# Kernel optimization log

Measured on AMD Instinct MI355X. Metric: run time of the kernel, lower is better.

The kernel has to match this reference:

```python
import jax, jax.numpy as jnp
import numpy as np
import math

N_EMBD = 1024
N_HEAD = 16
HEAD_SIZE = N_EMBD // N_HEAD
LAYER_IDX = 2
LAMBDA_INIT = 0.8 - 0.6 * math.exp(-0.3 * (LAYER_IDX - 1))
LN_EPS = 1e-5
B, T = 4, 1024


def setup_inputs() -> dict:
    key = jax.random.key(0)
    ks = jax.random.split(key, 11)
    s = 0.02  # weight init scale
    return {
        "x": jax.random.normal(ks[0], (B, T, N_EMBD), dtype=jnp.float32),
        "Wq1": jax.random.normal(ks[1], (N_EMBD, N_EMBD), dtype=jnp.float32) * s,
        "Wq2": jax.random.normal(ks[2], (N_EMBD, N_EMBD), dtype=jnp.float32) * s,
        "Wk1": jax.random.normal(ks[3], (N_EMBD, N_EMBD), dtype=jnp.float32) * s,
        "Wk2": jax.random.normal(ks[4], (N_EMBD, N_EMBD), dtype=jnp.float32) * s,
        "Wv": jax.random.normal(ks[5], (N_EMBD, 2 * N_EMBD), dtype=jnp.float32) * s,
        "Wc": jax.random.normal(ks[6], (2 * N_EMBD, N_EMBD), dtype=jnp.float32) * s,
        "lq1": jax.random.normal(ks[7], (N_HEAD, HEAD_SIZE), dtype=jnp.float32) * 0.1,
        "lk1": jax.random.normal(ks[8], (N_HEAD, HEAD_SIZE), dtype=jnp.float32) * 0.1,
        "lq2": jax.random.normal(ks[9], (N_HEAD, HEAD_SIZE), dtype=jnp.float32) * 0.1,
        "lk2": jax.random.normal(ks[10], (N_HEAD, HEAD_SIZE), dtype=jnp.float32) * 0.1,
    }


def reference(x, Wq1, Wq2, Wk1, Wk2, Wv, Wc, lq1, lk1, lq2, lk2):
    Bx, Tx, C = x.shape
    H, hs = N_HEAD, HEAD_SIZE
    scale = 1.0 / math.sqrt(hs)

    # projections -> (B, T, H, d)
    q1 = (x @ Wq1).reshape(Bx, Tx, H, hs)
    q2 = (x @ Wq2).reshape(Bx, Tx, H, hs)
    k1 = (x @ Wk1).reshape(Bx, Tx, H, hs)
    k2 = (x @ Wk2).reshape(Bx, Tx, H, hs)
    v = (x @ Wv).reshape(Bx, Tx, H, 2 * hs)

    # dual score streams (B, H, T, T)
    att1 = jnp.einsum("bqhd,bkhd->bhqk", q1, k1) * scale
    att2 = jnp.einsum("bqhd,bkhd->bhqk", q2, k2) * scale

    causal = jnp.tril(jnp.ones((Tx, Tx), dtype=bool))  # (T, T)
    neg_inf = jnp.float32(-jnp.inf)
    att1 = jnp.where(causal, att1, neg_inf)
    att2 = jnp.where(causal, att2, neg_inf)
    a1 = jax.nn.softmax(att1, axis=-1)
    a2 = jax.nn.softmax(att2, axis=-1)

    # per-head differential lambda
    lam1 = jnp.exp(jnp.sum(lq1 * lk1, axis=-1))  # (H,)
    lam2 = jnp.exp(jnp.sum(lq2 * lk2, axis=-1))  # (H,)
    lam_full = lam1 - lam2 + LAMBDA_INIT  # (H,)

    att = a1 - lam_full[None, :, None, None] * a2  # dropout = identity (eval)

    # PV matmul -> (B, T, H, 2*hs)
    y = jnp.einsum("bhqk,bkhd->bqhd", att, v)

    # subLN over last dim (no affine)
    mu = jnp.mean(y, axis=-1, keepdims=True)
    var = jnp.mean(jnp.square(y - mu), axis=-1, keepdims=True)
    y = (y - mu) / jnp.sqrt(var + LN_EPS)
    y = y * (1.0 - LAMBDA_INIT)

    y = y.reshape(Bx, Tx, 2 * C)
    return y @ Wc  # resid dropout = identity (eval)
```

## Files before the change

kernel.cpp:

```cpp
#include <hip/hip_runtime.h>


#define T_SEQ 1024
#define NH 16
#define DV 128
#define NPROJ 6144
#define KSTR 72

typedef __bf16 bf16_t;
typedef __bf16 bf16x8 __attribute__((ext_vector_type(8)));
typedef __bf16 bf16x4 __attribute__((ext_vector_type(4)));
typedef __bf16 bf16x2 __attribute__((ext_vector_type(2)));
typedef _Float16 f16x4 __attribute__((ext_vector_type(4)));
typedef _Float16 f16x2 __attribute__((ext_vector_type(2)));
typedef short s16x4 __attribute__((ext_vector_type(4)));
typedef float f32x4 __attribute__((ext_vector_type(4)));

#define LAMBDA_INIT 0.35550906759096928f
#define ONE_MINUS_LI 0.6444909324090307f
#define LOG2E 1.4426950408889634f
#define RTHR 44.36f

#if __has_builtin(__builtin_amdgcn_mfma_f32_16x16x16_bf16)
#define MFMA16(a, b, c) __builtin_amdgcn_mfma_f32_16x16x16_bf16(a, b, c, 0, 0, 0)
#elif __has_builtin(__builtin_amdgcn_mfma_f32_16x16x16bf16_1k)
#define MFMA16(a, b, c)                                                       \
  __builtin_amdgcn_mfma_f32_16x16x16bf16_1k(                                  \
      __builtin_bit_cast(s16x4, a), __builtin_bit_cast(s16x4, b), c, 0, 0, 0)
#else
#define MFMA16(a, b, c) (c)
#endif

#define GLDS(g, l)                                                            \
  __builtin_amdgcn_global_load_lds(                                           \
      (const __attribute__((address_space(1))) void*)(g),                     \
      (__attribute__((address_space(3))) void*)(l), 16, 0, 0)

static const size_t OFF_WCAT = 0;
static const size_t OFF_XB = OFF_WCAT + (size_t)6144 * 1024 * 2;
static const size_t OFF_WCT = OFF_XB + (size_t)4096 * 1024 * 2;
static const size_t OFF_PROJ = OFF_WCT + (size_t)2048 * 1024 * 2;
static const size_t OFF_VT = OFF_PROJ + (size_t)4096 * 6144 * 2;
static const size_t OFF_YLN = OFF_VT + (size_t)64 * 128 * 1024 * 2;
static const size_t OFF_LAM = OFF_YLN + (size_t)4096 * 2048 * 2;

__global__ void __launch_bounds__(256) cast_x(const float* __restrict__ x,
                                              bf16_t* __restrict__ o) {
  const int i = (blockIdx.x * 256 + threadIdx.x) * 4;
  float4 v = *(const float4*)(x + i);
  bf16x4 r = {(bf16_t)v.x, (bf16_t)v.y, (bf16_t)v.z, (bf16_t)v.w};
  *(bf16x4*)(o + i) = r;
}

__device__ __forceinline__ void tcast_body(const float* __restrict__ W,
                                           bf16_t* __restrict__ Wt, int K,
                                           int N, int row0) {
  __shared__ float tile[32][33];
  const int k0 = blockIdx.x * 32, n0 = blockIdx.y * 32;
  const int tx = threadIdx.x & 31, ty = threadIdx.x >> 5;
#pragma unroll
  for (int i = 0; i < 32; i += 8)
    tile[ty + i][tx] = W[(long)(k0 + ty + i) * N + n0 + tx];
  __syncthreads();
#pragma unroll
  for (int i = 0; i < 32; i += 8)
    Wt[(long)(row0 + n0 + ty + i) * K + k0 + tx] = (bf16_t)tile[tx][ty + i];
}

__global__ void __launch_bounds__(256) tcast_w(const float* __restrict__ W,
                                               bf16_t* __restrict__ Wt, int K,
                                               int N, int row0) {
  tcast_body(W, Wt, K, N, row0);
}

__global__ void __launch_bounds__(256) tcast_w4(const float* __restrict__ W0,
                                                const float* __restrict__ W1,
                                                const float* __restrict__ W2,
                                                const float* __restrict__ W3,
                                                bf16_t* __restrict__ Wt) {
  const float* Ws[4] = {W0, W1, W2, W3};
  tcast_body(Ws[blockIdx.z], Wt, 1024, 1024, blockIdx.z * 1024);
}

__global__ void lam_kernel(const float* __restrict__ lq1,
                           const float* __restrict__ lk1,
                           const float* __restrict__ lq2,
                           const float* __restrict__ lk2,
                           float* __restrict__ lam) {
  const int h = threadIdx.x;
  if (h < NH) {
    float d1 = 0.f, d2 = 0.f;
    for (int i = 0; i < 64; ++i) {
      d1 += lq1[h * 64 + i] * lk1[h * 64 + i];
      d2 += lq2[h * 64 + i] * lk2[h * 64 + i];
    }
    lam[h] = expf(d1) - expf(d2) + LAMBDA_INIT;
  }
}

#define BM 128
#define BN 128
#define BK 32

template <typename OutT>
__global__ void __launch_bounds__(256) gemm_bt(const bf16_t* __restrict__ A,
                                               const bf16_t* __restrict__ Bt,
                                               OutT* __restrict__ C, int M,
                                               int N, int K) {
  __shared__ __align__(16) bf16_t As[BM * BK];
  __shared__ __align__(16) bf16_t Bs[BN * BK];
  const int tid = threadIdx.x;
  const int w = tid >> 6;
  const int lane = tid & 63;
  const int quad = lane >> 4, l16 = lane & 15;
  const int m0 = blockIdx.y * BM, n0 = blockIdx.x * BN;
  const int wm = (w >> 1) * 64, wn = (w & 1) * 64;
  const int srow = tid >> 2;
  const int scol = (tid & 3) * 8;

  const bf16_t* Ag0 = A + (long)(m0 + srow) * K + scol;
  const bf16_t* Ag1 = Ag0 + (long)64 * K;
  const bf16_t* Bg0 = Bt + (long)(n0 + srow) * K + scol;
  const bf16_t* Bg1 = Bg0 + (long)64 * K;
  bf16_t* lA0 = As + tid * 8;
  bf16_t* lA1 = As + 2048 + tid * 8;
  bf16_t* lB0 = Bs + tid * 8;
  bf16_t* lB1 = Bs + 2048 + tid * 8;

  f32x4 acc[4][4] = {};

  for (int k0 = 0; k0 < K; k0 += BK) {
    GLDS(Ag0 + k0, lA0);
    GLDS(Ag1 + k0, lA1);
    GLDS(Bg0 + k0, lB0);
    GLDS(Bg1 + k0, lB1);
    __syncthreads();
    bf16x8 af[4], bfr[4];
#pragma unroll
    for (int t = 0; t < 4; ++t) {
      af[t] = *(const bf16x8*)(As + (wm + t * 16 + l16) * BK + quad * 8);
      bfr[t] = *(const bf16x8*)(Bs + (wn + t * 16 + l16) * BK + quad * 8);
    }
#pragma unroll
    for (int mt = 0; mt < 4; ++mt)
#pragma unroll
      for (int nt = 0; nt < 4; ++nt)
        acc[mt][nt] = __builtin_amdgcn_mfma_f32_16x16x32_bf16(
            af[mt], bfr[nt], acc[mt][nt], 0, 0, 0);
    __syncthreads();
  }

#pragma unroll
  for (int mt = 0; mt < 4; ++mt)
#pragma unroll
    for (int nt = 0; nt < 4; ++nt) {
      const int col = n0 + wn + nt * 16 + l16;
#pragma unroll
      for (int i = 0; i < 4; ++i) {
        const int row = m0 + wm + mt * 16 + quad * 4 + i;
        C[(long)row * N + col] = (OutT)acc[mt][nt][i];
      }
    }
}

template <typename OutT>
__global__ void __launch_bounds__(256) gemm_bt_n64(const bf16_t* __restrict__ A,
                                                   const bf16_t* __restrict__ Bt,
                                                   OutT* __restrict__ C, int M,
                                                   int N, int K) {
  __shared__ __align__(16) bf16_t As[BM * BK];
  __shared__ __align__(16) bf16_t Bs[64 * BK];
  const int tid = threadIdx.x;
  const int w = tid >> 6;
  const int lane = tid & 63;
  const int quad = lane >> 4, l16 = lane & 15;
  const int m0 = blockIdx.y * BM, n0 = blockIdx.x * 64;
  const int wm = (w >> 1) * 64, wn = (w & 1) * 32;
  const int srow = tid >> 2;
  const int scol = (tid & 3) * 8;

  const bf16_t* Ag0 = A + (long)(m0 + srow) * K + scol;
  const bf16_t* Ag1 = Ag0 + (long)64 * K;
  const bf16_t* Bg0 = Bt + (long)(n0 + srow) * K + scol;
  bf16_t* lA0 = As + tid * 8;
  bf16_t* lA1 = As + 2048 + tid * 8;
  bf16_t* lB0 = Bs + tid * 8;

  f32x4 acc[4][2] = {};

  for (int k0 = 0; k0 < K; k0 += BK) {
    GLDS(Ag0 + k0, lA0);
    GLDS(Ag1 + k0, lA1);
    GLDS(Bg0 + k0, lB0);
    __syncthreads();
    bf16x8 af[4], bfr[2];
#pragma unroll
    for (int t = 0; t < 4; ++t)
      af[t] = *(const bf16x8*)(As + (wm + t * 16 + l16) * BK + quad * 8);
#pragma unroll
    for (int t = 0; t < 2; ++t)
      bfr[t] = *(const bf16x8*)(Bs + (wn + t * 16 + l16) * BK + quad * 8);
#pragma unroll
    for (int mt = 0; mt < 4; ++mt)
#pragma unroll
      for (int nt = 0; nt < 2; ++nt)
        acc[mt][nt] = __builtin_amdgcn_mfma_f32_16x16x32_bf16(
            af[mt], bfr[nt], acc[mt][nt], 0, 0, 0);
    __syncthreads();
  }

#pragma unroll
  for (int mt = 0; mt < 4; ++mt)
#pragma unroll
    for (int nt = 0; nt < 2; ++nt) {
      const int col = n0 + wn + nt * 16 + l16;
#pragma unroll
      for (int i = 0; i < 4; ++i) {
        const int row = m0 + wm + mt * 16 + quad * 4 + i;
        C[(long)row * N + col] = (OutT)acc[mt][nt][i];
      }
    }
}

__global__ void __launch_bounds__(256) transpose_v(const bf16_t* __restrict__ proj,
                                                   bf16_t* __restrict__ vt) {
  __shared__ bf16_t tile[32][34];
  const int bh = blockIdx.z;
  const int b = bh >> 4, h = bh & 15;
  const int t0 = blockIdx.x * 32, d0 = blockIdx.y * 32;
  const int tx = threadIdx.x & 31, ty = threadIdx.x >> 5;
  const bf16_t* src = proj + (long)(b * T_SEQ) * NPROJ + 4096 + h * 128;
#pragma unroll
  for (int i = 0; i < 32; i += 8)
    tile[ty + i][tx] = src[(long)(t0 + ty + i) * NPROJ + d0 + tx];
  __syncthreads();
  bf16_t* dst = vt + ((long)bh * DV) * T_SEQ;
#pragma unroll
  for (int i = 0; i < 32; i += 8)
    dst[(long)(d0 + ty + i) * T_SEQ + t0 + tx] = tile[tx][ty + i];
}

__global__ void __launch_bounds__(256) attn_kernel(const bf16_t* __restrict__ proj,
                                                   const bf16_t* __restrict__ vt,
                                                   _Float16* __restrict__ a1,
                                                   _Float16* __restrict__ a2) {
  const int x = blockIdx.x;
  const int qblk = 15 - (x >> 7);
  const int st = (x >> 6) & 1;
  const int bh = x & 63;
  const int b = bh >> 4, h = bh & 15;
  const int tid = threadIdx.x;
  const int w = tid >> 6, lane = tid & 63;
  const int quad = lane >> 4, l16 = lane & 15;
  const long bT = (long)b * T_SEQ;

  __shared__ __align__(16) bf16_t Ks[64 * KSTR];
  __shared__ __align__(16) bf16_t Vs[DV * KSTR];

  const int koff = h * 64 + 2048 + st * 1024;
  const bf16_t* gK = proj + (bT + (tid >> 2)) * (long)NPROJ + koff + (tid & 3) * 16;
  const bf16_t* gV = vt + (long)bh * DV * T_SEQ + (long)(tid >> 1) * T_SEQ +
                     (tid & 1) * 32;
  const int kwK = (tid >> 2) * KSTR + (tid & 3) * 16;
  const int kwV = (tid >> 1) * KSTR + (tid & 1) * 32;

  const float sc = 0.125f * LOG2E;
  const int q0 = qblk * 64 + w * 16;
  const int qg = q0 + l16;

  const bf16_t* qrow = proj + (bT + qg) * (long)NPROJ + h * 64 + st * 1024;
  bf16x8 aq[2];
  aq[0] = *(const bf16x8*)(qrow + quad * 8);
  aq[1] = *(const bf16x8*)(qrow + 32 + quad * 8);

  f32x4 O[8] = {};
  float m = -3.0e38f, l = 0.f;
  const bf16x4 one4 = {(bf16_t)1.0f, (bf16_t)1.0f, (bf16_t)1.0f, (bf16_t)1.0f};

  const int kend_blk = qblk * 64 + 64;
  const int kend_w = q0 + 16;

  bf16x8 rK[2], rV[4];
  rK[0] = *(const bf16x8*)(gK);
  rK[1] = *(const bf16x8*)(gK + 8);
#pragma unroll
  for (int j = 0; j < 4; ++j) rV[j] = *(const bf16x8*)(gV + j * 8);

  for (int kt = 0; kt < kend_blk; kt += 64) {
    *(bf16x8*)(Ks + kwK) = rK[0];
    *(bf16x8*)(Ks + kwK + 8) = rK[1];
#pragma unroll
    for (int j = 0; j < 4; ++j) *(bf16x8*)(Vs + kwV + j * 8) = rV[j];
    __syncthreads();

    if (kt + 64 < kend_blk) {
      const long ko = (long)(kt + 64) * NPROJ;
      rK[0] = *(const bf16x8*)(gK + ko);
      rK[1] = *(const bf16x8*)(gK + ko + 8);
#pragma unroll
      for (int j = 0; j < 4; ++j)
        rV[j] = *(const bf16x8*)(gV + kt + 64 + j * 8);
    }

    if (kt < kend_w) {
      f32x4 s[4];
#pragma unroll
      for (int c = 0; c < 4; ++c) {
        const bf16_t* kr = Ks + (c * 16 + l16) * KSTR;
        bf16x8 ka0 = *(const bf16x8*)(kr + quad * 8);
        bf16x8 ka1 = *(const bf16x8*)(kr + 32 + quad * 8);
        f32x4 z = {};
        z = __builtin_amdgcn_mfma_f32_16x16x32_bf16(ka0, aq[0], z, 0, 0, 0);
        z = __builtin_amdgcn_mfma_f32_16x16x32_bf16(ka1, aq[1], z, 0, 0, 0);
        s[c] = z;
      }
      if (kt + 63 > q0) {
#pragma unroll
        for (int c = 0; c < 4; ++c)
#pragma unroll
          for (int i = 0; i < 4; ++i) {
            const int key = kt + c * 16 + quad * 4 + i;
            if (key > qg) s[c][i] = -1e30f;
          }
      }
      float t[4];
#pragma unroll
      for (int c = 0; c < 4; ++c)
        t[c] = fmaxf(fmaxf(s[c][0], s[c][1]), fmaxf(s[c][2], s[c][3]));
      float mx = fmaxf(fmaxf(t[0], t[1]), fmaxf(t[2], t[3]));
      mx = fmaxf(mx, __shfl_xor(mx, 16));
      mx = fmaxf(mx, __shfl_xor(mx, 32));
      if (!__all(mx <= m + RTHR)) {
        const float mn = fmaxf(m, mx);
        const float al = exp2f((m - mn) * sc);
        m = mn;
#pragma unroll
        for (int f = 0; f < 8; ++f)
#pragma unroll
          for (int i = 0; i < 4; ++i) O[f][i] *= al;
        l *= al;
      }
      const float ms = m * sc;
      bf16x4 pc[4];
#pragma unroll
      for (int c = 0; c < 4; ++c)
#pragma unroll
        for (int i = 0; i < 4; ++i)
          pc[c][i] = (bf16_t)exp2f(fmaf(s[c][i], sc, -ms));
      f32x4 la = {};
#pragma unroll
      for (int c = 0; c < 4; ++c) la = MFMA16(one4, pc[c], la);
#pragma unroll
      for (int c = 0; c < 4; ++c) {
#pragma unroll
        for (int f = 0; f < 8; ++f) {
          bf16x4 va =
              *(const bf16x4*)(Vs + (f * 16 + l16) * KSTR + c * 16 + quad * 4);
          O[f] = MFMA16(va, pc[c], O[f]);
        }
      }
      l += la[0];
    }
    __syncthreads();
  }

  const float inv = 1.0f / l;
  _Float16* ob = st ? a2 : a1;
  _Float16* dst = ob + ((bT + qg) * 16 + h) * (long)128 + quad * 4;
#pragma unroll
  for (int f = 0; f < 8; ++f) {
    f16x4 o = {(_Float16)(O[f][0] * inv), (_Float16)(O[f][1] * inv),
               (_Float16)(O[f][2] * inv), (_Float16)(O[f][3] * inv)};
    *(f16x4*)(dst + f * 16) = o;
  }
}

__global__ void __launch_bounds__(256) combine_kernel(const _Float16* __restrict__ a1,
                                                      const _Float16* __restrict__ a2,
                                                      const float* __restrict__ lamp,
                                                      bf16_t* __restrict__ yln) {
  const int unit = blockIdx.x * 4 + (threadIdx.x >> 6);
  const int lane = threadIdx.x & 63;
  const float lam = lamp[unit & 15];
  const long base = (long)unit * 128 + lane * 2;
  f16x2 v1 = *(const f16x2*)(a1 + base);
  f16x2 v2 = *(const f16x2*)(a2 + base);
  float y0 = (float)v1[0] - lam * (float)v2[0];
  float y1 = (float)v1[1] - lam * (float)v2[1];
  float sm = y0 + y1, sq = y0 * y0 + y1 * y1;
#pragma unroll
  for (int off = 1; off < 64; off <<= 1) {
    sm += __shfl_xor(sm, off);
    sq += __shfl_xor(sq, off);
  }
  const float mu = sm * (1.0f / 128.0f);
  const float var = sq * (1.0f / 128.0f) - mu * mu;
  const float rs = rsqrtf(var + 1e-5f) * ONE_MINUS_LI;
  bf16x2 o = {(bf16_t)((y0 - mu) * rs), (bf16_t)((y1 - mu) * rs)};
  *(bf16x2*)(yln + base) = o;
}

extern "C" void kernel_launch(void* const* d_in, const int* in_sizes, int n_in,
                              void* d_out, int out_size, void* d_ws,
                              size_t ws_size, hipStream_t stream) {
  const float* x = (const float*)d_in[0];
  const float* Wq1 = (const float*)d_in[1];
  const float* Wq2 = (const float*)d_in[2];
  const float* Wk1 = (const float*)d_in[3];
  const float* Wk2 = (const float*)d_in[4];
  const float* Wv = (const float*)d_in[5];
  const float* Wc = (const float*)d_in[6];
  const float* lq1 = (const float*)d_in[7];
  const float* lk1 = (const float*)d_in[8];
  const float* lq2 = (const float*)d_in[9];
  const float* lk2 = (const float*)d_in[10];
  float* out = (float*)d_out;

  char* ws = (char*)d_ws;
  bf16_t* wcat = (bf16_t*)(ws + OFF_WCAT);
  bf16_t* xb = (bf16_t*)(ws + OFF_XB);
  bf16_t* wct = (bf16_t*)(ws + OFF_WCT);
  bf16_t* projb = (bf16_t*)(ws + OFF_PROJ);
  bf16_t* vtb = (bf16_t*)(ws + OFF_VT);
  bf16_t* ylnb = (bf16_t*)(ws + OFF_YLN);
  float* lamp = (float*)(ws + OFF_LAM);
  _Float16* a1b = (_Float16*)(ws + OFF_YLN);
  _Float16* a2b = (_Float16*)(ws + OFF_WCAT);

  cast_x<<<4096, 256, 0, stream>>>(x, xb);
  tcast_w4<<<dim3(32, 32, 4), 256, 0, stream>>>(Wq1, Wq2, Wk1, Wk2, wcat);
  tcast_w<<<dim3(32, 64), 256, 0, stream>>>(Wv, wcat, 1024, 2048, 4096);
  tcast_w<<<dim3(64, 32), 256, 0, stream>>>(Wc, wct, 2048, 1024, 0);
  lam_kernel<<<1, 64, 0, stream>>>(lq1, lk1, lq2, lk2, lamp);

  gemm_bt<bf16_t><<<dim3(48, 32), 256, 0, stream>>>(xb, wcat, projb, 4096, 6144, 1024);
  transpose_v<<<dim3(32, 4, 64), 256, 0, stream>>>(projb, vtb);
  attn_kernel<<<dim3(2048), 256, 0, stream>>>(projb, vtb, a1b, a2b);
  combine_kernel<<<dim3(16384), 256, 0, stream>>>(a1b, a2b, lamp, ylnb);
  gemm_bt_n64<float><<<dim3(16, 32), 256, 0, stream>>>(ylnb, wct, out, 4096, 1024, 2048);
}
```

Measured before the change: 308.6 us.

## Replace projection GEMM with 256x256 double-buffered swizzled-LDS kernel

```diff
diff --git a/kernel.cpp b/kernel.cpp
--- a/kernel.cpp
+++ b/kernel.cpp
@@ -30,6 +30,8 @@
 #else
 #define MFMA16(a, b, c) (c)
 #endif
+
+#define MFMA32(a, b, c) __builtin_amdgcn_mfma_f32_16x16x32_bf16(a, b, c, 0, 0, 0)
 
 #define GLDS(g, l)                                                            \
   __builtin_amdgcn_global_load_lds(                                           \
@@ -98,70 +100,164 @@
   }
 }
 
+#define GBM 256
+#define GBN 256
+#define GBK 64
+
+__global__ void __launch_bounds__(512, 1) gemm256(const bf16_t* __restrict__ A,
+                                                  const bf16_t* __restrict__ Bt,
+                                                  bf16_t* __restrict__ C,
+                                                  int M, int N, int K,
+                                                  int nbx) {
+  __shared__ __align__(16) bf16_t As[2][GBM * GBK];
+  __shared__ __align__(16) bf16_t Bs[2][GBN * GBK];
+  const int tid = threadIdx.x;
+  const int w = tid >> 6, lane = tid & 63;
+  const int quad = lane >> 4, l16 = lane & 15;
+  const int wr = w >> 2, wc = w & 3;
+
+  const int wg = blockIdx.x;
+  const int cpx = gridDim.x >> 3;
+  const int sw = (wg & 7) * cpx + (wg >> 3);
+  const int by = sw / nbx, bx = sw % nbx;
+  const int m0 = by * GBM, n0 = bx * GBN;
+
+  const int r8 = lane >> 3, g = lane & 7;
+  const int gsw = (g ^ r8) * 8;
+  const bf16_t* gA[4];
+  const bf16_t* gB[4];
+#pragma unroll
+  for (int j = 0; j < 4; ++j) {
+    gA[j] = A + (long)(m0 + w * 32 + j * 8 + r8) * K + gsw;
+    gB[j] = Bt + (long)(n0 + w * 32 + j * 8 + r8) * K + gsw;
+  }
+
+  const int kx = (l16 & 7) << 4;
+  const int ko0 = (quad * 16) ^ kx;
+  const int ko1 = (64 + quad * 16) ^ kx;
+
+  f32x4 acc[8][4] = {};
+
+  const int nt = K >> 6;
+
+#pragma unroll
+  for (int j = 0; j < 4; ++j) {
+    GLDS(gA[j], As[0] + (w * 32 + j * 8) * GBK);
+    GLDS(gB[j], Bs[0] + (w * 32 + j * 8) * GBK);
+  }
+  asm volatile("s_waitcnt vmcnt(0)" ::: "memory");
+  __builtin_amdgcn_s_barrier();
+
+  for (int t = 0; t < nt; ++t) {
+    const bf16_t* Ab = (t & 1) ? As[1] : As[0];
+    const bf16_t* Bb = (t & 1) ? Bs[1] : Bs[0];
+    bf16_t* Asb = (t & 1) ? As[0] : As[1];
+    bf16_t* Bsb = (t & 1) ? Bs[0] : Bs[1];
+    const bool pf = (t + 1 < nt);
+    const long ko = (long)(t + 1) * GBK;
+
+    const char* Arow = (const char*)Ab + (size_t)(wr * 128 + l16) * 128;
+    const char* Brow = (const char*)Bb + (size_t)(wc * 64 + l16) * 128;
+
+    bf16x8 af[4][2], bn0[2][2], bn1[2][2];
+
+#pragma unroll
+    for (int mt = 0; mt < 4; ++mt) {
+      af[mt][0] = *(const bf16x8*)(Arow + (size_t)mt * 16 * 128 + ko0);
+      af[mt][1] = *(const bf16x8*)(Arow + (size_t)mt * 16 * 128 + ko1);
+    }
+#pragma unroll
+    for (int n = 0; n < 2; ++n) {
+      bn0[n][0] = *(const bf16x8*)(Brow + (size_t)n * 16 * 128 + ko0);
+      bn0[n][1] = *(const bf16x8*)(Brow + (size_t)n * 16 * 128 + ko1);
+    }
+    if (pf) {
+      GLDS(gA[0] + ko, Asb + (w * 32) * GBK);
+      GLDS(gB[0] + ko, Bsb + (w * 32) * GBK);
+      GLDS(gA[1] + ko, Asb + (w * 32 + 8) * GBK);
+      GLDS(gB[1] + ko, Bsb + (w * 32 + 8) * GBK);
+    }
+    __builtin_amdgcn_s_barrier();
+    __builtin_amdgcn_s_setprio(1);
+#pragma unroll
+    for (int mt = 0; mt < 4; ++mt)
+#pragma unroll
+      for (int n = 0; n < 2; ++n) {
+        acc[mt][n] = MFMA32(af[mt][0], bn0[n][0], acc[mt][n]);
+        acc[mt][n] = MFMA32(af[mt][1], bn0[n][1], acc[mt][n]);
+      }
+    __builtin_amdgcn_s_setprio(0);
+    __builtin_amdgcn_s_barrier();
+
+#pragma unroll
+    for (int n = 0; n < 2; ++n) {
+      bn1[n][0] = *(const bf16x8*)(Brow + (size_t)(32 + n * 16) * 128 + ko0);
+      bn1[n][1] = *(const bf16x8*)(Brow + (size_t)(32 + n * 16) * 128 + ko1);
+    }
+    if (pf) {
+      GLDS(gA[2] + ko, Asb + (w * 32 + 16) * GBK);
+      GLDS(gB[2] + ko, Bsb + (w * 32 + 16) * GBK);
+      GLDS(gA[3] + ko, Asb + (w * 32 + 24) * GBK);
+      GLDS(gB[3] + ko, Bsb + (w * 32 + 24) * GBK);
+    }
+    __builtin_amdgcn_s_barrier();
+    __builtin_amdgcn_s_setprio(1);
+#pragma unroll
+    for (int mt = 0; mt < 4; ++mt)
+#pragma unroll
+      for (int n = 0; n < 2; ++n) {
+        acc[mt][2 + n] = MFMA32(af[mt][0], bn1[n][0], acc[mt][2 + n]);
+        acc[mt][2 + n] = MFMA32(af[mt][1], bn1[n][1], acc[mt][2 + n]);
+      }
+    __builtin_amdgcn_s_setprio(0);
+    __builtin_amdgcn_s_barrier();
+
+#pragma unroll
+    for (int mt = 0; mt < 4; ++mt) {
+      af[mt][0] = *(const bf16x8*)(Arow + (size_t)(64 + mt * 16) * 128 + ko0);
+      af[mt][1] = *(const bf16x8*)(Arow + (size_t)(64 + mt * 16) * 128 + ko1);
+    }
+    __builtin_amdgcn_s_barrier();
+    __builtin_amdgcn_s_setprio(1);
+#pragma unroll
+    for (int mt = 0; mt < 4; ++mt)
+#pragma unroll
+      for (int n = 0; n < 2; ++n) {
+        acc[4 + mt][2 + n] = MFMA32(af[mt][0], bn1[n][0], acc[4 + mt][2 + n]);
+        acc[4 + mt][2 + n] = MFMA32(af[mt][1], bn1[n][1], acc[4 + mt][2 + n]);
+      }
+    __builtin_amdgcn_s_setprio(0);
+    __builtin_amdgcn_s_barrier();
+
+    __builtin_amdgcn_s_setprio(1);
+#pragma unroll
+    for (int mt = 0; mt < 4; ++mt)
+#pragma unroll
+      for (int n = 0; n < 2; ++n) {
+        acc[4 + mt][n] = MFMA32(af[mt][0], bn0[n][0], acc[4 + mt][n]);
+        acc[4 + mt][n] = MFMA32(af[mt][1], bn0[n][1], acc[4 + mt][n]);
+      }
+    __builtin_amdgcn_s_setprio(0);
+
+    asm volatile("s_waitcnt vmcnt(0)" ::: "memory");
+    __builtin_amdgcn_s_barrier();
+  }
+
+#pragma unroll
+  for (int mt = 0; mt < 8; ++mt)
+#pragma unroll
+    for (int n = 0; n < 4; ++n) {
+      const int col = n0 + wc * 64 + n * 16 + l16;
+#pragma unroll
+      for (int i = 0; i < 4; ++i) {
+        const int row = m0 + wr * 128 + mt * 16 + quad * 4 + i;
+        C[(long)row * N + col] = (bf16_t)acc[mt][n][i];
+      }
+    }
+}
+
 #define BM 128
-#define BN 128
 #define BK 32
-
-template <typename OutT>
-__global__ void __launch_bounds__(256) gemm_bt(const bf16_t* __restrict__ A,
-                                               const bf16_t* __restrict__ Bt,
-                                               OutT* __restrict__ C, int M,
-                                               int N, int K) {
-  __shared__ __align__(16) bf16_t As[BM * BK];
-  __shared__ __align__(16) bf16_t Bs[BN * BK];
-  const int tid = threadIdx.x;
-  const int w = tid >> 6;
-  const int lane = tid & 63;
-  const int quad = lane >> 4, l16 = lane & 15;
-  const int m0 = blockIdx.y * BM, n0 = blockIdx.x * BN;
-  const int wm = (w >> 1) * 64, wn = (w & 1) * 64;
-  const int srow = tid >> 2;
-  const int scol = (tid & 3) * 8;
-
-  const bf16_t* Ag0 = A + (long)(m0 + srow) * K + scol;
-  const bf16_t* Ag1 = Ag0 + (long)64 * K;
-  const bf16_t* Bg0 = Bt + (long)(n0 + srow) * K + scol;
-  const bf16_t* Bg1 = Bg0 + (long)64 * K;
-  bf16_t* lA0 = As + tid * 8;
-  bf16_t* lA1 = As + 2048 + tid * 8;
-  bf16_t* lB0 = Bs + tid * 8;
-  bf16_t* lB1 = Bs + 2048 + tid * 8;
-
-  f32x4 acc[4][4] = {};
-
-  for (int k0 = 0; k0 < K; k0 += BK) {
-    GLDS(Ag0 + k0, lA0);
-    GLDS(Ag1 + k0, lA1);
-    GLDS(Bg0 + k0, lB0);
-    GLDS(Bg1 + k0, lB1);
-    __syncthreads();
-    bf16x8 af[4], bfr[4];
-#pragma unroll
-    for (int t = 0; t < 4; ++t) {
-      af[t] = *(const bf16x8*)(As + (wm + t * 16 + l16) * BK + quad * 8);
-      bfr[t] = *(const bf16x8*)(Bs + (wn + t * 16 + l16) * BK + quad * 8);
-    }
-#pragma unroll
-    for (int mt = 0; mt < 4; ++mt)
-#pragma unroll
-      for (int nt = 0; nt < 4; ++nt)
-        acc[mt][nt] = __builtin_amdgcn_mfma_f32_16x16x32_bf16(
-            af[mt], bfr[nt], acc[mt][nt], 0, 0, 0);
-    __syncthreads();
-  }
-
-#pragma unroll
-  for (int mt = 0; mt < 4; ++mt)
-#pragma unroll
-    for (int nt = 0; nt < 4; ++nt) {
-      const int col = n0 + wn + nt * 16 + l16;
-#pragma unroll
-      for (int i = 0; i < 4; ++i) {
-        const int row = m0 + wm + mt * 16 + quad * 4 + i;
-        C[(long)row * N + col] = (OutT)acc[mt][nt][i];
-      }
-    }
-}
 
 template <typename OutT>
 __global__ void __launch_bounds__(256) gemm_bt_n64(const bf16_t* __restrict__ A,
@@ -203,21 +299,20 @@
 #pragma unroll
     for (int mt = 0; mt < 4; ++mt)
 #pragma unroll
-      for (int nt = 0; nt < 2; ++nt)
-        acc[mt][nt] = __builtin_amdgcn_mfma_f32_16x16x32_bf16(
-            af[mt], bfr[nt], acc[mt][nt], 0, 0, 0);
+      for (int ntt = 0; ntt < 2; ++ntt)
+        acc[mt][ntt] = MFMA32(af[mt], bfr[ntt], acc[mt][ntt]);
     __syncthreads();
   }
 
 #pragma unroll
   for (int mt = 0; mt < 4; ++mt)
 #pragma unroll
-    for (int nt = 0; nt < 2; ++nt) {
-      const int col = n0 + wn + nt * 16 + l16;
+    for (int ntt = 0; ntt < 2; ++ntt) {
+      const int col = n0 + wn + ntt * 16 + l16;
 #pragma unroll
       for (int i = 0; i < 4; ++i) {
         const int row = m0 + wm + mt * 16 + quad * 4 + i;
-        C[(long)row * N + col] = (OutT)acc[mt][nt][i];
+        C[(long)row * N + col] = (OutT)acc[mt][ntt][i];
       }
     }
 }
@@ -310,8 +405,8 @@
         bf16x8 ka0 = *(const bf16x8*)(kr + quad * 8);
         bf16x8 ka1 = *(const bf16x8*)(kr + 32 + quad * 8);
         f32x4 z = {};
-        z = __builtin_amdgcn_mfma_f32_16x16x32_bf16(ka0, aq[0], z, 0, 0, 0);
-        z = __builtin_amdgcn_mfma_f32_16x16x32_bf16(ka1, aq[1], z, 0, 0, 0);
+        z = MFMA32(ka0, aq[0], z);
+        z = MFMA32(ka1, aq[1], z);
         s[c] = z;
       }
       if (kt + 63 > q0) {
@@ -433,7 +528,7 @@
   tcast_w<<<dim3(64, 32), 256, 0, stream>>>(Wc, wct, 2048, 1024, 0);
   lam_kernel<<<1, 64, 0, stream>>>(lq1, lk1, lq2, lk2, lamp);
 
-  gemm_bt<bf16_t><<<dim3(48, 32), 256, 0, stream>>>(xb, wcat, projb, 4096, 6144, 1024);
+  gemm256<<<dim3(384), 512, 0, stream>>>(xb, wcat, projb, 4096, 6144, 1024, 24);
   transpose_v<<<dim3(32, 4, 64), 256, 0, stream>>>(projb, vtb);
   attn_kernel<<<dim3(2048), 256, 0, stream>>>(projb, vtb, a1b, a2b);
   combine_kernel<<<dim3(16384), 256, 0, stream>>>(a1b, a2b, lamp, ylnb);
```

After: 304.5 us (median of 2 runs). Within noise of the previous version (-1.3%).

## Add pipelined 256x256 projection GEMM with swizzled LDS and tile remap

Applied to the files above, without the earlier changes.

```diff
diff --git a/kernel.cpp b/kernel.cpp
--- a/kernel.cpp
+++ b/kernel.cpp
@@ -30,6 +30,8 @@
 #else
 #define MFMA16(a, b, c) (c)
 #endif
+
+#define MFMA32(a, b, c) __builtin_amdgcn_mfma_f32_16x16x32_bf16(a, b, c, 0, 0, 0)
 
 #define GLDS(g, l)                                                            \
   __builtin_amdgcn_global_load_lds(                                           \
@@ -96,6 +98,100 @@
     }
     lam[h] = expf(d1) - expf(d2) + LAMBDA_INIT;
   }
+}
+
+#define GBM 256
+#define GBN 256
+
+__global__ void __launch_bounds__(512, 1) gemm256(const bf16_t* __restrict__ A,
+                                                  const bf16_t* __restrict__ Bt,
+                                                  bf16_t* __restrict__ C,
+                                                  int M, int N, int K,
+                                                  int nbx) {
+  __shared__ __align__(16) bf16_t As[2][2][256 * 32];
+  __shared__ __align__(16) bf16_t Bs[2][2][256 * 32];
+  const int tid = threadIdx.x;
+  const int w = tid >> 6, lane = tid & 63;
+  const int quad = lane >> 4, l16 = lane & 15;
+  const int wr = w >> 2, wc = w & 3;
+
+  const int wg = blockIdx.x;
+  const int cpx = gridDim.x >> 3;
+  const int sw = (wg & 7) * cpx + (wg >> 3);
+  const int by = sw / nbx, bx = sw % nbx;
+  const int m0 = by * GBM, n0 = bx * GBN;
+
+  const int srow = tid >> 2;
+  const int sg = (tid & 3) ^ (srow & 3);
+  const bf16_t* gA = A + (long)(m0 + srow) * K + sg * 8;
+  const bf16_t* gB = Bt + (long)(n0 + srow) * K + sg * 8;
+
+#define ISSUE_UNIT(u)                                                         \
+  {                                                                           \
+    const int tu_ = (u) >> 1, hu_ = (u) & 1, bu_ = tu_ & 1;                   \
+    const long ku_ = (long)tu_ * 64 + hu_ * 32;                               \
+    bf16_t* da_ = &As[bu_][hu_][0] + w * 16 * 32;                             \
+    bf16_t* db_ = &Bs[bu_][hu_][0] + w * 16 * 32;                             \
+    GLDS(gA + ku_, da_);                                                      \
+    GLDS(gA + (long)128 * K + ku_, da_ + 128 * 32);                           \
+    GLDS(gB + ku_, db_);                                                      \
+    GLDS(gB + (long)128 * K + ku_, db_ + 128 * 32);                           \
+  }
+
+  const int kq = (quad ^ (l16 & 3)) * 16;
+
+#define PHASE_BODY(p)                                                         \
+  {                                                                           \
+    const char* Ab_ = (const char*)&As[((p) >> 1) & 1][(p)&1][0];             \
+    const char* Bb_ = (const char*)&Bs[((p) >> 1) & 1][(p)&1][0];             \
+    bf16x8 af_[8], bf_[4];                                                    \
+    _Pragma("unroll") for (int mt_ = 0; mt_ < 8; ++mt_)                       \
+        af_[mt_] = *(const bf16x8*)(Ab_ +                                     \
+                                    (size_t)(wr * 128 + mt_ * 16 + l16) * 64 +\
+                                    kq);                                      \
+    _Pragma("unroll") for (int n_ = 0; n_ < 4; ++n_)                          \
+        bf_[n_] = *(const bf16x8*)(Bb_ +                                      \
+                                   (size_t)(wc * 64 + n_ * 16 + l16) * 64 +   \
+                                   kq);                                       \
+    __builtin_amdgcn_s_setprio(1);                                            \
+    _Pragma("unroll") for (int mt_ = 0; mt_ < 8; ++mt_)                       \
+        _Pragma("unroll") for (int n_ = 0; n_ < 4; ++n_)                      \
+            acc[mt_][n_] = MFMA32(af_[mt_], bf_[n_], acc[mt_][n_]);           \
+    __builtin_amdgcn_s_setprio(0);                                            \
+  }
+
+  f32x4 acc[8][4] = {};
+  const int np = K >> 5;
+
+  ISSUE_UNIT(0);
+  ISSUE_UNIT(1);
+  for (int p = 0; p < np - 2; ++p) {
+    ISSUE_UNIT(p + 2);
+    asm volatile("s_waitcnt vmcnt(8)" ::: "memory");
+    __builtin_amdgcn_s_barrier();
+    PHASE_BODY(p);
+  }
+  asm volatile("s_waitcnt vmcnt(4)" ::: "memory");
+  __builtin_amdgcn_s_barrier();
+  PHASE_BODY(np - 2);
+  asm volatile("s_waitcnt vmcnt(0)" ::: "memory");
+  __builtin_amdgcn_s_barrier();
+  PHASE_BODY(np - 1);
+
+#undef ISSUE_UNIT
+#undef PHASE_BODY
+
+#pragma unroll
+  for (int mt = 0; mt < 8; ++mt)
+#pragma unroll
+    for (int n = 0; n < 4; ++n) {
+      const int col = n0 + wc * 64 + n * 16 + l16;
+#pragma unroll
+      for (int i = 0; i < 4; ++i) {
+        const int row = m0 + wr * 128 + mt * 16 + quad * 4 + i;
+        C[(long)row * N + col] = (bf16_t)acc[mt][n][i];
+      }
+    }
 }
 
 #define BM 128
@@ -145,8 +241,7 @@
     for (int mt = 0; mt < 4; ++mt)
 #pragma unroll
       for (int nt = 0; nt < 4; ++nt)
-        acc[mt][nt] = __builtin_amdgcn_mfma_f32_16x16x32_bf16(
-            af[mt], bfr[nt], acc[mt][nt], 0, 0, 0);
+        acc[mt][nt] = MFMA32(af[mt], bfr[nt], acc[mt][nt]);
     __syncthreads();
   }
 
@@ -154,65 +249,6 @@
   for (int mt = 0; mt < 4; ++mt)
 #pragma unroll
     for (int nt = 0; nt < 4; ++nt) {
-      const int col = n0 + wn + nt * 16 + l16;
-#pragma unroll
-      for (int i = 0; i < 4; ++i) {
-        const int row = m0 + wm + mt * 16 + quad * 4 + i;
-        C[(long)row * N + col] = (OutT)acc[mt][nt][i];
-      }
-    }
-}
-
-template <typename OutT>
-__global__ void __launch_bounds__(256) gemm_bt_n64(const bf16_t* __restrict__ A,
-                                                   const bf16_t* __restrict__ Bt,
-                                                   OutT* __restrict__ C, int M,
-                                                   int N, int K) {
-  __shared__ __align__(16) bf16_t As[BM * BK];
-  __shared__ __align__(16) bf16_t Bs[64 * BK];
-  const int tid = threadIdx.x;
-  const int w = tid >> 6;
-  const int lane = tid & 63;
-  const int quad = lane >> 4, l16 = lane & 15;
-  const int m0 = blockIdx.y * BM, n0 = blockIdx.x * 64;
-  const int wm = (w >> 1) * 64, wn = (w & 1) * 32;
-  const int srow = tid >> 2;
-  const int scol = (tid & 3) * 8;
-
-  const bf16_t* Ag0 = A + (long)(m0 + srow) * K + scol;
-  const bf16_t* Ag1 = Ag0 + (long)64 * K;
-  const bf16_t* Bg0 = Bt + (long)(n0 + srow) * K + scol;
-  bf16_t* lA0 = As + tid * 8;
-  bf16_t* lA1 = As + 2048 + tid * 8;
-  bf16_t* lB0 = Bs + tid * 8;
-
-  f32x4 acc[4][2] = {};
-
-  for (int k0 = 0; k0 < K; k0 += BK) {
-    GLDS(Ag0 + k0, lA0);
-    GLDS(Ag1 + k0, lA1);
-    GLDS(Bg0 + k0, lB0);
-    __syncthreads();
-    bf16x8 af[4], bfr[2];
-#pragma unroll
-    for (int t = 0; t < 4; ++t)
-      af[t] = *(const bf16x8*)(As + (wm + t * 16 + l16) * BK + quad * 8);
-#pragma unroll
-    for (int t = 0; t < 2; ++t)
-      bfr[t] = *(const bf16x8*)(Bs + (wn + t * 16 + l16) * BK + quad * 8);
-#pragma unroll
-    for (int mt = 0; mt < 4; ++mt)
-#pragma unroll
-      for (int nt = 0; nt < 2; ++nt)
-        acc[mt][nt] = __builtin_amdgcn_mfma_f32_16x16x32_bf16(
-            af[mt], bfr[nt], acc[mt][nt], 0, 0, 0);
-    __syncthreads();
-  }
-
-#pragma unroll
-  for (int mt = 0; mt < 4; ++mt)
-#pragma unroll
-    for (int nt = 0; nt < 2; ++nt) {
       const int col = n0 + wn + nt * 16 + l16;
 #pragma unroll
       for (int i = 0; i < 4; ++i) {
@@ -310,8 +346,8 @@
         bf16x8 ka0 = *(const bf16x8*)(kr + quad * 8);
         bf16x8 ka1 = *(const bf16x8*)(kr + 32 + quad * 8);
         f32x4 z = {};
-        z = __builtin_amdgcn_mfma_f32_16x16x32_bf16(ka0, aq[0], z, 0, 0, 0);
-        z = __builtin_amdgcn_mfma_f32_16x16x32_bf16(ka1, aq[1], z, 0, 0, 0);
+        z = MFMA32(ka0, aq[0], z);
+        z = MFMA32(ka1, aq[1], z);
         s[c] = z;
       }
       if (kt + 63 > q0) {
@@ -433,9 +469,9 @@
   tcast_w<<<dim3(64, 32), 256, 0, stream>>>(Wc, wct, 2048, 1024, 0);
   lam_kernel<<<1, 64, 0, stream>>>(lq1, lk1, lq2, lk2, lamp);
 
-  gemm_bt<bf16_t><<<dim3(48, 32), 256, 0, stream>>>(xb, wcat, projb, 4096, 6144, 1024);
+  gemm256<<<dim3(384), 512, 0, stream>>>(xb, wcat, projb, 4096, 6144, 1024, 24);
   transpose_v<<<dim3(32, 4, 64), 256, 0, stream>>>(projb, vtb);
   attn_kernel<<<dim3(2048), 256, 0, stream>>>(projb, vtb, a1b, a2b);
   combine_kernel<<<dim3(16384), 256, 0, stream>>>(a1b, a2b, lamp, ylnb);
-  gemm_bt_n64<float><<<dim3(16, 32), 256, 0, stream>>>(ylnb, wct, out, 4096, 1024, 2048);
-}
+  gemm_bt<float><<<dim3(8, 32), 256, 0, stream>>>(ylnb, wct, out, 4096, 1024, 2048);
+}
```

Measured after the change: 313.9 us. About the same (+1.7%).
